# Performance work log

Measured on AMD Instinct MI355X. Metric: run time of the kernel, lower is better.

## Reference

```python
import jax, jax.numpy as jnp
import numpy as np

N = 262144          # number of input vectors (flattened tokens)
K = 1024            # codebook_size
D = 64              # embedding_dim
DECAY = 0.99
EPS = 1e-5
COMMIT = 0.25


def setup_inputs() -> dict:
    key = jax.random.key(0)
    k1, k2 = jax.random.split(key, 2)
    inputs = jax.random.normal(k1, (N, D), dtype=jnp.float32)
    # codebook.weight.data.normal_() -> standard normal init
    codebook = jax.random.normal(k2, (K, D), dtype=jnp.float32)
    ema_cluster_size = jnp.zeros((K,), dtype=jnp.float32)
    ema_w = codebook  # registered buffer initialized to a clone of the codebook
    return {"inputs": inputs, "codebook": codebook,
            "ema_cluster_size": ema_cluster_size, "ema_w": ema_w}


def reference(inputs, codebook, ema_cluster_size, ema_w):
    distances = (jnp.sum(inputs ** 2, axis=1, keepdims=True)
                 + jnp.sum(codebook ** 2, axis=1)
                 - 2.0 * (inputs @ codebook.T))
    encoding_indices = jnp.argmin(distances, axis=1)          # [N]

    # one_hot @ codebook  ==  gather
    quantized = codebook[encoding_indices]                    # [N, D]

    # --- training-mode EMA codebook update (buffers, no gradients) ---
    # encodings.sum(0)  ==  per-code counts
    counts = jax.ops.segment_sum(jnp.ones((inputs.shape[0],), inputs.dtype),
                                 encoding_indices, num_segments=K)
    new_cluster_size = DECAY * ema_cluster_size + (1.0 - DECAY) * counts
    n = jnp.sum(new_cluster_size)
    smoothed_size = (new_cluster_size + EPS) / (n + K * EPS) * n
    # encodings.T @ inputs  ==  segment sum of inputs by assigned code
    dw = jax.ops.segment_sum(inputs, encoding_indices, num_segments=K)  # [K, D]
    new_ema_w = DECAY * ema_w + (1.0 - DECAY) * dw
    new_codebook = new_ema_w / smoothed_size[:, None]

    # Straight-through estimator
    quantized_st = inputs + jax.lax.stop_gradient(quantized - inputs)
    e_latent_loss = jnp.mean((jax.lax.stop_gradient(quantized_st) - inputs) ** 2)
    loss = COMMIT * e_latent_loss

    return quantized_st, loss, encoding_indices, new_codebook, new_cluster_size, new_ema_w
```

## Files before the change

kernel.cpp:

```cpp
#include <hip/hip_runtime.h>

#define NN 262144
#define KK 1024
#define DD 64
#define DECAY 0.99f
#define ONE_MINUS_DECAY 0.01f
#define EPSF 1e-5f
#define COMMIT 0.25f

#define ROWB 144
#define CHUNK_CODES 32
#define PLANE_BYTES (CHUNK_CODES * ROWB)
#define CHUNK_BYTES (PLANE_BYTES * 2)
#define NCHUNK (KK / CHUNK_CODES)
#define RBLK 16384
#define CBLK 64
#define ROWS_PER_CBLK (NN / CBLK)

typedef __bf16 bf16x8 __attribute__((ext_vector_type(8)));
typedef unsigned short ushort8 __attribute__((ext_vector_type(8)));
typedef float float4v __attribute__((ext_vector_type(4)));

__device__ inline unsigned short bf16rne(float f) {
    unsigned int u = __float_as_uint(f);
    u += 0x7fffu + ((u >> 16) & 1u);
    return (unsigned short)(u >> 16);
}

__device__ inline void glds16(const void* g, void* l) {
    __builtin_amdgcn_global_load_lds(
        (const __attribute__((address_space(1))) unsigned int*)g,
        (__attribute__((address_space(3))) unsigned int*)l, 16, 0, 0);
}

__global__ __launch_bounds__(256) void k_prep(const float* __restrict__ cb,
                                              unsigned char* __restrict__ cbhl,
                                              float* __restrict__ csq_half,
                                              float* __restrict__ dw) {
    int e = blockIdx.x * 256 + threadIdx.x;
    dw[e] = 0.f;
    int k = e >> 6, d = e & 63;
    int c = k >> 5, kl = k & 31;
    float f = cb[e];
    unsigned short h = bf16rne(f);
    float hf = __uint_as_float((unsigned int)h << 16);
    unsigned short l = bf16rne(f - hf);
    unsigned char* base = cbhl + (size_t)c * CHUNK_BYTES;
    *(unsigned short*)(base + kl * ROWB + d * 2) = h;
    *(unsigned short*)(base + PLANE_BYTES + kl * ROWB + d * 2) = l;
    float s = f * f;
#pragma unroll
    for (int off = 32; off > 0; off >>= 1) s += __shfl_down(s, off);
    if (d == 0) csq_half[k] = 0.5f * s;
}

__global__ __launch_bounds__(256, 4) void k_assign(
    const float* __restrict__ x,
    const unsigned char* __restrict__ cbhl, const float* __restrict__ csq_half,
    int* __restrict__ kkpack)
{
    __shared__ __align__(16) unsigned char ldsbuf[2][CHUNK_BYTES];

    const int tid  = threadIdx.x;
    const int lane = tid & 63;
    const int wave = tid >> 6;
    const int col  = lane & 15;
    const int quad = lane >> 4;
    const int rowbase = blockIdx.x * 128 + wave * 32;

    {
        const unsigned char* src = cbhl;
#pragma unroll
        for (int i = 0; i < 2; ++i) {
            int off = (i * 256 + tid) * 16;
            glds16(src + off, &ldsbuf[0][off]);
        }
        if (tid < 64) {
            int off = 8192 + tid * 16;
            glds16(src + off, &ldsbuf[0][off]);
        }
    }

    bf16x8 nah[2][2], nal[2][2];
    float xsq1[8];
    {
        float xsqm[2];
#pragma unroll
        for (int mt = 0; mt < 2; ++mt) {
            const float* xb = x + (size_t)(rowbase + mt * 16 + col) * DD + quad * 8;
            float s = 0.f;
#pragma unroll
            for (int kh = 0; kh < 2; ++kh) {
                float4 f0 = *(const float4*)(xb + kh * 32);
                float4 f1 = *(const float4*)(xb + kh * 32 + 4);
                s += f0.x * f0.x + f0.y * f0.y + f0.z * f0.z + f0.w * f0.w;
                s += f1.x * f1.x + f1.y * f1.y + f1.z * f1.z + f1.w * f1.w;
                float fv[8] = {f0.x, f0.y, f0.z, f0.w, f1.x, f1.y, f1.z, f1.w};
                ushort8 uh, ul;
#pragma unroll
                for (int j = 0; j < 8; ++j) {
                    float nf = -fv[j];
                    unsigned short h = bf16rne(nf);
                    float hf = __uint_as_float((unsigned int)h << 16);
                    uh[j] = h;
                    ul[j] = bf16rne(nf - hf);
                }
                nah[mt][kh] = __builtin_bit_cast(bf16x8, uh);
                nal[mt][kh] = __builtin_bit_cast(bf16x8, ul);
            }
            s += __shfl_xor(s, 16);
            s += __shfl_xor(s, 32);
            xsqm[mt] = s;
        }
#pragma unroll
        for (int mt = 0; mt < 2; ++mt)
#pragma unroll
            for (int r = 0; r < 4; ++r)
                xsq1[mt * 4 + r] = 0.5f * __shfl(xsqm[mt], quad * 4 + r) + 1.0f;
    }

    unsigned int best[8], sec[8];
#pragma unroll
    for (int j = 0; j < 8; ++j) { best[j] = 0xFFFFFFFFu; sec[j] = 0xFFFFFFFFu; }

    asm volatile("s_waitcnt vmcnt(0) lgkmcnt(0)" ::: "memory");
    __builtin_amdgcn_s_barrier();

    for (int chunk = 0; chunk < NCHUNK; ++chunk) {
        const unsigned char* cbuf = ldsbuf[chunk & 1];
        if (chunk + 1 < NCHUNK) {
            unsigned char* nbuf = ldsbuf[(chunk + 1) & 1];
            const unsigned char* src = cbhl + (size_t)(chunk + 1) * CHUNK_BYTES;
#pragma unroll
            for (int i = 0; i < 2; ++i) {
                int off = (i * 256 + tid) * 16;
                glds16(src + off, nbuf + off);
            }
            if (tid < 64) {
                int off = 8192 + tid * 16;
                glds16(src + off, nbuf + off);
            }
        }

        float csqv[2];
#pragma unroll
        for (int ct = 0; ct < 2; ++ct)
            csqv[ct] = csq_half[chunk * CHUNK_CODES + ct * 16 + col];

#pragma unroll
        for (int ct = 0; ct < CHUNK_CODES / 16; ++ct) {
            const int code_local = ct * 16 + col;
            const unsigned int codeCol = chunk * CHUNK_CODES + code_local;
            const unsigned char* bp = cbuf + code_local * ROWB + quad * 16;
            bf16x8 bh0 = __builtin_bit_cast(bf16x8, *(const uint4*)(bp));
            bf16x8 bh1 = __builtin_bit_cast(bf16x8, *(const uint4*)(bp + 64));
            bf16x8 bl0 = __builtin_bit_cast(bf16x8, *(const uint4*)(bp + PLANE_BYTES));
            bf16x8 bl1 = __builtin_bit_cast(bf16x8, *(const uint4*)(bp + PLANE_BYTES + 64));
            float csq = csqv[ct];

#pragma unroll
            for (int mt = 0; mt < 2; ++mt) {
                float4v a = {csq + xsq1[mt * 4 + 0], csq + xsq1[mt * 4 + 1],
                             csq + xsq1[mt * 4 + 2], csq + xsq1[mt * 4 + 3]};
                __builtin_amdgcn_s_setprio(1);
                a = __builtin_amdgcn_mfma_f32_16x16x32_bf16(nah[mt][0], bh0, a, 0, 0, 0);
                a = __builtin_amdgcn_mfma_f32_16x16x32_bf16(nah[mt][1], bh1, a, 0, 0, 0);
                a = __builtin_amdgcn_mfma_f32_16x16x32_bf16(nah[mt][0], bl0, a, 0, 0, 0);
                a = __builtin_amdgcn_mfma_f32_16x16x32_bf16(nah[mt][1], bl1, a, 0, 0, 0);
                a = __builtin_amdgcn_mfma_f32_16x16x32_bf16(nal[mt][0], bh0, a, 0, 0, 0);
                a = __builtin_amdgcn_mfma_f32_16x16x32_bf16(nal[mt][1], bh1, a, 0, 0, 0);
                __builtin_amdgcn_s_setprio(0);
#pragma unroll
                for (int r = 0; r < 4; ++r) {
                    unsigned int u = (__float_as_uint(a[r]) & 0xFFFFFC00u) | codeCol;
                    unsigned int j = mt * 4 + r;
                    unsigned int s2;
                    asm("v_med3_u32 %0, %1, %2, %3"
                        : "=v"(s2) : "v"(best[j]), "v"(u), "v"(sec[j]));
                    sec[j] = s2;
                    best[j] = best[j] < u ? best[j] : u;
                }
            }
        }

        asm volatile("s_waitcnt vmcnt(0) lgkmcnt(0)" ::: "memory");
        __builtin_amdgcn_s_barrier();
    }

#pragma unroll
    for (int m = 1; m <= 8; m <<= 1) {
#pragma unroll
        for (int j = 0; j < 8; ++j) {
            unsigned int ob = __shfl_xor(best[j], m, 16);
            unsigned int os = __shfl_xor(sec[j],  m, 16);
            unsigned int hi = best[j] > ob ? best[j] : ob;
            best[j] = best[j] < ob ? best[j] : ob;
            unsigned int s2 = sec[j] < os ? sec[j] : os;
            sec[j] = s2 < hi ? s2 : hi;
        }
    }

    if (col == 0) {
#pragma unroll
        for (int j = 0; j < 8; ++j) {
            int row_local = (j >> 2) * 16 + quad * 4 + (j & 3);
            kkpack[rowbase + row_local] =
                (int)((best[j] & 1023u) | ((sec[j] & 1023u) << 10));
        }
    }
}

__global__ __launch_bounds__(256) void k_refine(
    const float* __restrict__ x, const float* __restrict__ cb,
    const float* __restrict__ csq_half, int* __restrict__ idx_io,
    float* __restrict__ quant, float* __restrict__ loss_parts)
{
    __shared__ float werr[4];
    const int tid  = threadIdx.x;
    const int lane = tid & 63;
    const int d16  = lane & 15;
    const int e    = blockIdx.x * 256 + tid;
    const int row  = e >> 4;

    unsigned int kp = (unsigned int)idx_io[row];
    int k1 = (int)(kp & 1023u), k2 = (int)((kp >> 10) & 1023u);

    float4 x4 = *(const float4*)(x + (size_t)row * DD + d16 * 4);
    float4 c1 = *(const float4*)(cb + (size_t)k1 * DD + d16 * 4);
    float4 c2 = *(const float4*)(cb + (size_t)k2 * DD + d16 * 4);

    float p1 = x4.x * c1.x + x4.y * c1.y + x4.z * c1.z + x4.w * c1.w;
    float p2 = x4.x * c2.x + x4.y * c2.y + x4.z * c2.z + x4.w * c2.w;
#pragma unroll
    for (int off = 1; off < 16; off <<= 1) {
        p1 += __shfl_xor(p1, off, 16);
        p2 += __shfl_xor(p2, off, 16);
    }
    float d1 = csq_half[k1] - p1;
    float d2 = csq_half[k2] - p2;
    bool pick1 = (d1 < d2) || (d1 == d2 && k1 < k2);
    int w = pick1 ? k1 : k2;
    float4 q = pick1 ? c1 : c2;

    *(float4*)(quant + (size_t)row * DD + d16 * 4) = q;

    float ex = q.x - x4.x, ey = q.y - x4.y, ez = q.z - x4.z, ew = q.w - x4.w;
    float err = ex * ex + ey * ey + ez * ez + ew * ew;
#pragma unroll
    for (int off = 32; off > 0; off >>= 1) err += __shfl_down(err, off);
    if (lane == 0) werr[tid >> 6] = err;
    __syncthreads();
    if (tid == 0)
        loss_parts[blockIdx.x] = werr[0] + werr[1] + werr[2] + werr[3];

    if (d16 == 0) idx_io[row] = w;
}

__global__ __launch_bounds__(1024) void k_count(
    const int* __restrict__ idx, int* __restrict__ counts_parts)
{
    __shared__ int hist[KK];
    const int tid = threadIdx.x;
    const int b   = blockIdx.x;
    hist[tid] = 0;
    __syncthreads();
    const int base = b * ROWS_PER_CBLK;
#pragma unroll
    for (int i = 0; i < ROWS_PER_CBLK / 1024; ++i)
        atomicAdd(&hist[idx[base + tid + i * 1024]], 1);
    __syncthreads();
    counts_parts[b * KK + tid] = hist[tid];
}

__global__ __launch_bounds__(1024) void k_mid(
    int* __restrict__ counts_parts, const float* __restrict__ ema_cs,
    const float* __restrict__ loss_parts,
    float* __restrict__ new_cs, float* __restrict__ loss_out,
    float* __restrict__ smoothed_inv)
{
    int t = threadIdx.x; int lane = t & 63; int w = t >> 6;

    __shared__ float wsumf[16];
    __shared__ int wsumi[16];
    __shared__ float wlp[16];
    __shared__ float ntot_s;

    float lp = 0.f;
#pragma unroll
    for (int i = 0; i < RBLK / 1024; ++i) lp += loss_parts[t + i * 1024];
#pragma unroll
    for (int off = 32; off > 0; off >>= 1) lp += __shfl_down(lp, off);
    if (lane == 0) wlp[w] = lp;

    int cnt = 0;
    for (int b = 0; b < CBLK; ++b) cnt += counts_parts[b * KK + t];
    float ncs = DECAY * ema_cs[t] + ONE_MINUS_DECAY * (float)cnt;

    float s = ncs;
#pragma unroll
    for (int off = 32; off > 0; off >>= 1) s += __shfl_down(s, off);
    if (lane == 0) wsumf[w] = s;

    int v = cnt;
#pragma unroll
    for (int off = 1; off < 64; off <<= 1) {
        int u = __shfl_up(v, off);
        if (lane >= off) v += u;
    }
    if (lane == 63) wsumi[w] = v;
    __syncthreads();
    if (t == 0) {
        float tt = 0.f, lt = 0.f;
        for (int i = 0; i < 16; ++i) { tt += wsumf[i]; lt += wlp[i]; }
        ntot_s = tt;
        loss_out[0] = COMMIT * lt / (float)(NN * DD);
    }
    if (w == 0 && lane < 16) {
        int u = wsumi[lane]; int vv = u;
#pragma unroll
        for (int off = 1; off < 16; off <<= 1) {
            int p = __shfl_up(vv, off, 16);
            if ((lane & 15) >= off) vv += p;
        }
        wsumi[lane] = vv - u;
    }
    __syncthreads();
    float n = ntot_s;

    float sm = (ncs + EPSF) / (n + (float)KK * EPSF) * n;
    new_cs[t] = ncs;
    smoothed_inv[t] = 1.0f / sm;

    int run = wsumi[w] + v - cnt;
    for (int b = 0; b < CBLK; ++b) {
        int c = counts_parts[b * KK + t];
        counts_parts[b * KK + t] = run;
        run += c;
    }
}

__global__ __launch_bounds__(1024) void k_scatter(
    int* __restrict__ idx_inout, const int* __restrict__ base_parts,
    int2* __restrict__ pairs)
{
    __shared__ int cur[KK];
    const int tid = threadIdx.x;
    const int b   = blockIdx.x;
    cur[tid] = base_parts[b * KK + tid];
    __syncthreads();
    const int base = b * ROWS_PER_CBLK;
#pragma unroll
    for (int i = 0; i < ROWS_PER_CBLK / 1024; ++i) {
        int r = base + tid + i * 1024;
        int k = idx_inout[r];
        int pos = atomicAdd(&cur[k], 1);
        pairs[pos] = make_int2(r, k);
        ((float*)idx_inout)[r] = (float)k;
    }
}

__global__ __launch_bounds__(256) void k_segsum(
    const float* __restrict__ x, const int2* __restrict__ pairs,
    float* __restrict__ dw)
{
    int w = blockIdx.x * 4 + (threadIdx.x >> 6);
    int lane = threadIdx.x & 63;
    int base = w * 64;
    int2 mine = pairs[base + lane];
    float acc = 0.f;
    int cur = __shfl(mine.y, 0);
    for (int rb = 0; rb < 64; rb += 8) {
        float v[8];
        int codes[8];
#pragma unroll
        for (int j = 0; j < 8; ++j) {
            int row  = __shfl(mine.x, rb + j);
            codes[j] = __shfl(mine.y, rb + j);
            v[j] = x[(size_t)row * DD + lane];
        }
#pragma unroll
        for (int j = 0; j < 8; ++j) {
            if (codes[j] != cur) {
                atomicAdd(&dw[cur * DD + lane], acc);
                acc = 0.f; cur = codes[j];
            }
            acc += v[j];
        }
    }
    atomicAdd(&dw[cur * DD + lane], acc);
}

__global__ __launch_bounds__(256) void k_final(
    const float* __restrict__ dw, const float* __restrict__ ema_w,
    const float* __restrict__ smoothed_inv,
    float* __restrict__ new_ema_w, float* __restrict__ new_cb)
{
    int i = blockIdx.x * 256 + threadIdx.x;
    int k = i >> 6;
    float nw = DECAY * ema_w[i] + ONE_MINUS_DECAY * dw[i];
    new_ema_w[i] = nw;
    new_cb[i] = nw * smoothed_inv[k];
}

extern "C" void kernel_launch(void* const* d_in, const int* in_sizes, int n_in,
                              void* d_out, int out_size, void* d_ws, size_t ws_size,
                              hipStream_t stream)
{
    const float* x      = (const float*)d_in[0];
    const float* cb     = (const float*)d_in[1];
    const float* ema_cs = (const float*)d_in[2];
    const float* ema_w  = (const float*)d_in[3];

    float* out      = (float*)d_out;
    float* quant    = out;
    float* loss_out = out + (size_t)NN * DD;
    int*   idx_reg  = (int*)(out + (size_t)NN * DD + 1);
    float* new_cb   = out + (size_t)NN * DD + 1 + NN;
    float* new_cs   = new_cb + (size_t)KK * DD;
    float* new_emaw = new_cs + KK;

    char* ws = (char*)d_ws;
    float* dw           = (float*)(ws + 4352);
    float* csq_half     = (float*)(ws + 274688);
    float* smoothed_inv = (float*)(ws + 278784);
    unsigned char* cbhl = (unsigned char*)(ws + 282880);
    int2*  pairs        = (int2*)(ws + 577792);
    int*   counts_parts = (int*)(ws + 282880);
    float* loss_parts   = (float*)(ws + 577792);

    k_prep   <<<KK * DD / 256, 256, 0, stream>>>(cb, cbhl, csq_half, dw);
    k_assign <<<NN / 128, 256, 0, stream>>>(x, cbhl, csq_half, idx_reg);
    k_refine <<<RBLK, 256, 0, stream>>>(x, cb, csq_half, idx_reg, quant,
                                        loss_parts);
    k_count  <<<CBLK, 1024, 0, stream>>>(idx_reg, counts_parts);
    k_mid    <<<1, 1024, 0, stream>>>(counts_parts, ema_cs, loss_parts,
                                      new_cs, loss_out, smoothed_inv);
    k_scatter<<<CBLK, 1024, 0, stream>>>(idx_reg, counts_parts, pairs);
    k_segsum <<<NN / 256, 256, 0, stream>>>(x, pairs, dw);
    k_final  <<<KK * DD / 256, 256, 0, stream>>>(dw, ema_w, smoothed_inv,
                                                 new_emaw, new_cb);
}
```

Measured before the change: 251.8 us.

## Switch assignment GEMM to 32x32x16 MFMA with MFMA-native codebook layout

Replaces the 16x16x32 bf16 MFMA tiling of the distance computation with 32x32x16 MFMAs. Each wave now covers 32 rows by 32 codes per chunk using 12 MFMAs on a 16-register accumulator. The codebook prep kernel writes the split-bf16 planes in a layout that matches the MFMA operand order, so each lane loads its fragments with contiguous 16-byte LDS reads and the padded rows go away. The change also drops the occupancy hint from the launch bounds, and the larger best/second-best state (16 registers each) raises register pressure.

New measurement: 270.0 us. 7.2% more time.

```diff
diff --git a/kernel.cpp b/kernel.cpp
--- a/kernel.cpp
+++ b/kernel.cpp
@@ -8,10 +8,9 @@
 #define EPSF 1e-5f
 #define COMMIT 0.25f
 
-#define ROWB 144
 #define CHUNK_CODES 32
-#define PLANE_BYTES (CHUNK_CODES * ROWB)
-#define CHUNK_BYTES (PLANE_BYTES * 2)
+#define PLANE_BYTES 4096
+#define CHUNK_BYTES 8192
 #define NCHUNK (KK / CHUNK_CODES)
 #define RBLK 16384
 #define CBLK 64
@@ -19,7 +18,7 @@
 
 typedef __bf16 bf16x8 __attribute__((ext_vector_type(8)));
 typedef unsigned short ushort8 __attribute__((ext_vector_type(8)));
-typedef float float4v __attribute__((ext_vector_type(4)));
+typedef float f32x16 __attribute__((ext_vector_type(16)));
 
 __device__ inline unsigned short bf16rne(float f) {
     unsigned int u = __float_as_uint(f);
@@ -40,21 +39,23 @@
     int e = blockIdx.x * 256 + threadIdx.x;
     dw[e] = 0.f;
     int k = e >> 6, d = e & 63;
-    int c = k >> 5, kl = k & 31;
+    int c = k >> 5, cl = k & 31;
+    int kb = d >> 4, hh = (d >> 3) & 1, j = d & 7;
     float f = cb[e];
-    unsigned short h = bf16rne(f);
-    float hf = __uint_as_float((unsigned int)h << 16);
-    unsigned short l = bf16rne(f - hf);
+    unsigned short h16 = bf16rne(f);
+    float hf = __uint_as_float((unsigned int)h16 << 16);
+    unsigned short l16 = bf16rne(f - hf);
     unsigned char* base = cbhl + (size_t)c * CHUNK_BYTES;
-    *(unsigned short*)(base + kl * ROWB + d * 2) = h;
-    *(unsigned short*)(base + PLANE_BYTES + kl * ROWB + d * 2) = l;
+    int off = kb * 1024 + hh * 512 + cl * 16 + j * 2;
+    *(unsigned short*)(base + off) = h16;
+    *(unsigned short*)(base + PLANE_BYTES + off) = l16;
     float s = f * f;
 #pragma unroll
-    for (int off = 32; off > 0; off >>= 1) s += __shfl_down(s, off);
+    for (int offr = 32; offr > 0; offr >>= 1) s += __shfl_down(s, offr);
     if (d == 0) csq_half[k] = 0.5f * s;
 }
 
-__global__ __launch_bounds__(256, 4) void k_assign(
+__global__ __launch_bounds__(256) void k_assign(
     const float* __restrict__ x,
     const unsigned char* __restrict__ cbhl, const float* __restrict__ csq_half,
     int* __restrict__ kkpack)
@@ -64,8 +65,8 @@
     const int tid  = threadIdx.x;
     const int lane = tid & 63;
     const int wave = tid >> 6;
-    const int col  = lane & 15;
-    const int quad = lane >> 4;
+    const int col  = lane & 31;
+    const int h    = lane >> 5;
     const int rowbase = blockIdx.x * 128 + wave * 32;
 
     {
@@ -75,53 +76,43 @@
             int off = (i * 256 + tid) * 16;
             glds16(src + off, &ldsbuf[0][off]);
         }
-        if (tid < 64) {
-            int off = 8192 + tid * 16;
-            glds16(src + off, &ldsbuf[0][off]);
-        }
-    }
-
-    bf16x8 nah[2][2], nal[2][2];
-    float xsq1[8];
+    }
+
+    bf16x8 nah[4], nal[4];
+    float xsq1[16];
     {
-        float xsqm[2];
-#pragma unroll
-        for (int mt = 0; mt < 2; ++mt) {
-            const float* xb = x + (size_t)(rowbase + mt * 16 + col) * DD + quad * 8;
-            float s = 0.f;
-#pragma unroll
-            for (int kh = 0; kh < 2; ++kh) {
-                float4 f0 = *(const float4*)(xb + kh * 32);
-                float4 f1 = *(const float4*)(xb + kh * 32 + 4);
-                s += f0.x * f0.x + f0.y * f0.y + f0.z * f0.z + f0.w * f0.w;
-                s += f1.x * f1.x + f1.y * f1.y + f1.z * f1.z + f1.w * f1.w;
-                float fv[8] = {f0.x, f0.y, f0.z, f0.w, f1.x, f1.y, f1.z, f1.w};
-                ushort8 uh, ul;
-#pragma unroll
-                for (int j = 0; j < 8; ++j) {
-                    float nf = -fv[j];
-                    unsigned short h = bf16rne(nf);
-                    float hf = __uint_as_float((unsigned int)h << 16);
-                    uh[j] = h;
-                    ul[j] = bf16rne(nf - hf);
-                }
-                nah[mt][kh] = __builtin_bit_cast(bf16x8, uh);
-                nal[mt][kh] = __builtin_bit_cast(bf16x8, ul);
+        const float* xr = x + (size_t)(rowbase + col) * DD + h * 8;
+        float s = 0.f;
+#pragma unroll
+        for (int kb = 0; kb < 4; ++kb) {
+            float4 f0 = *(const float4*)(xr + kb * 16);
+            float4 f1 = *(const float4*)(xr + kb * 16 + 4);
+            s += f0.x * f0.x + f0.y * f0.y + f0.z * f0.z + f0.w * f0.w;
+            s += f1.x * f1.x + f1.y * f1.y + f1.z * f1.z + f1.w * f1.w;
+            float fv[8] = {f0.x, f0.y, f0.z, f0.w, f1.x, f1.y, f1.z, f1.w};
+            ushort8 uh, ul;
+#pragma unroll
+            for (int j = 0; j < 8; ++j) {
+                float nf = -fv[j];
+                unsigned short hb = bf16rne(nf);
+                float hf = __uint_as_float((unsigned int)hb << 16);
+                uh[j] = hb;
+                ul[j] = bf16rne(nf - hf);
             }
-            s += __shfl_xor(s, 16);
-            s += __shfl_xor(s, 32);
-            xsqm[mt] = s;
-        }
-#pragma unroll
-        for (int mt = 0; mt < 2; ++mt)
-#pragma unroll
-            for (int r = 0; r < 4; ++r)
-                xsq1[mt * 4 + r] = 0.5f * __shfl(xsqm[mt], quad * 4 + r) + 1.0f;
-    }
-
-    unsigned int best[8], sec[8];
-#pragma unroll
-    for (int j = 0; j < 8; ++j) { best[j] = 0xFFFFFFFFu; sec[j] = 0xFFFFFFFFu; }
+            nah[kb] = __builtin_bit_cast(bf16x8, uh);
+            nal[kb] = __builtin_bit_cast(bf16x8, ul);
+        }
+        s += __shfl_xor(s, 32);
+#pragma unroll
+        for (int reg = 0; reg < 16; ++reg) {
+            int R = (reg & 3) + 8 * (reg >> 2) + 4 * h;
+            xsq1[reg] = 0.5f * __shfl(s, R) + 1.0f;
+        }
+    }
+
+    unsigned int best[16], sec[16];
+#pragma unroll
+    for (int j = 0; j < 16; ++j) { best[j] = 0xFFFFFFFFu; sec[j] = 0xFFFFFFFFu; }
 
     asm volatile("s_waitcnt vmcnt(0) lgkmcnt(0)" ::: "memory");
     __builtin_amdgcn_s_barrier();
@@ -136,51 +127,44 @@
                 int off = (i * 256 + tid) * 16;
                 glds16(src + off, nbuf + off);
             }
-            if (tid < 64) {
-                int off = 8192 + tid * 16;
-                glds16(src + off, nbuf + off);
-            }
-        }
-
-        float csqv[2];
-#pragma unroll
-        for (int ct = 0; ct < 2; ++ct)
-            csqv[ct] = csq_half[chunk * CHUNK_CODES + ct * 16 + col];
-
-#pragma unroll
-        for (int ct = 0; ct < CHUNK_CODES / 16; ++ct) {
-            const int code_local = ct * 16 + col;
-            const unsigned int codeCol = chunk * CHUNK_CODES + code_local;
-            const unsigned char* bp = cbuf + code_local * ROWB + quad * 16;
-            bf16x8 bh0 = __builtin_bit_cast(bf16x8, *(const uint4*)(bp));
-            bf16x8 bh1 = __builtin_bit_cast(bf16x8, *(const uint4*)(bp + 64));
-            bf16x8 bl0 = __builtin_bit_cast(bf16x8, *(const uint4*)(bp + PLANE_BYTES));
-            bf16x8 bl1 = __builtin_bit_cast(bf16x8, *(const uint4*)(bp + PLANE_BYTES + 64));
-            float csq = csqv[ct];
-
-#pragma unroll
-            for (int mt = 0; mt < 2; ++mt) {
-                float4v a = {csq + xsq1[mt * 4 + 0], csq + xsq1[mt * 4 + 1],
-                             csq + xsq1[mt * 4 + 2], csq + xsq1[mt * 4 + 3]};
-                __builtin_amdgcn_s_setprio(1);
-                a = __builtin_amdgcn_mfma_f32_16x16x32_bf16(nah[mt][0], bh0, a, 0, 0, 0);
-                a = __builtin_amdgcn_mfma_f32_16x16x32_bf16(nah[mt][1], bh1, a, 0, 0, 0);
-                a = __builtin_amdgcn_mfma_f32_16x16x32_bf16(nah[mt][0], bl0, a, 0, 0, 0);
-                a = __builtin_amdgcn_mfma_f32_16x16x32_bf16(nah[mt][1], bl1, a, 0, 0, 0);
-                a = __builtin_amdgcn_mfma_f32_16x16x32_bf16(nal[mt][0], bh0, a, 0, 0, 0);
-                a = __builtin_amdgcn_mfma_f32_16x16x32_bf16(nal[mt][1], bh1, a, 0, 0, 0);
-                __builtin_amdgcn_s_setprio(0);
-#pragma unroll
-                for (int r = 0; r < 4; ++r) {
-                    unsigned int u = (__float_as_uint(a[r]) & 0xFFFFFC00u) | codeCol;
-                    unsigned int j = mt * 4 + r;
-                    unsigned int s2;
-                    asm("v_med3_u32 %0, %1, %2, %3"
-                        : "=v"(s2) : "v"(best[j]), "v"(u), "v"(sec[j]));
-                    sec[j] = s2;
-                    best[j] = best[j] < u ? best[j] : u;
-                }
-            }
+        }
+
+        float csq = csq_half[chunk * CHUNK_CODES + col];
+        const unsigned int codeCol = chunk * CHUNK_CODES + col;
+
+        bf16x8 bh[4], bl[4];
+#pragma unroll
+        for (int kb = 0; kb < 4; ++kb) {
+            bh[kb] = __builtin_bit_cast(bf16x8,
+                *(const uint4*)(cbuf + kb * 1024 + lane * 16));
+            bl[kb] = __builtin_bit_cast(bf16x8,
+                *(const uint4*)(cbuf + PLANE_BYTES + kb * 1024 + lane * 16));
+        }
+
+        f32x16 a;
+#pragma unroll
+        for (int reg = 0; reg < 16; ++reg) a[reg] = csq + xsq1[reg];
+
+        __builtin_amdgcn_s_setprio(1);
+#pragma unroll
+        for (int kb = 0; kb < 4; ++kb)
+            a = __builtin_amdgcn_mfma_f32_32x32x16_bf16(nah[kb], bh[kb], a, 0, 0, 0);
+#pragma unroll
+        for (int kb = 0; kb < 4; ++kb)
+            a = __builtin_amdgcn_mfma_f32_32x32x16_bf16(nah[kb], bl[kb], a, 0, 0, 0);
+#pragma unroll
+        for (int kb = 0; kb < 4; ++kb)
+            a = __builtin_amdgcn_mfma_f32_32x32x16_bf16(nal[kb], bh[kb], a, 0, 0, 0);
+        __builtin_amdgcn_s_setprio(0);
+
+#pragma unroll
+        for (int reg = 0; reg < 16; ++reg) {
+            unsigned int u = (__float_as_uint(a[reg]) & 0xFFFFFC00u) | codeCol;
+            unsigned int s2;
+            asm("v_med3_u32 %0, %1, %2, %3"
+                : "=v"(s2) : "v"(best[reg]), "v"(u), "v"(sec[reg]));
+            sec[reg] = s2;
+            best[reg] = best[reg] < u ? best[reg] : u;
         }
 
         asm volatile("s_waitcnt vmcnt(0) lgkmcnt(0)" ::: "memory");
@@ -188,24 +172,24 @@
     }
 
 #pragma unroll
-    for (int m = 1; m <= 8; m <<= 1) {
-#pragma unroll
-        for (int j = 0; j < 8; ++j) {
-            unsigned int ob = __shfl_xor(best[j], m, 16);
-            unsigned int os = __shfl_xor(sec[j],  m, 16);
-            unsigned int hi = best[j] > ob ? best[j] : ob;
-            best[j] = best[j] < ob ? best[j] : ob;
-            unsigned int s2 = sec[j] < os ? sec[j] : os;
-            sec[j] = s2 < hi ? s2 : hi;
+    for (int m = 1; m <= 16; m <<= 1) {
+#pragma unroll
+        for (int reg = 0; reg < 16; ++reg) {
+            unsigned int ob = __shfl_xor(best[reg], m);
+            unsigned int os = __shfl_xor(sec[reg], m);
+            unsigned int hi = best[reg] > ob ? best[reg] : ob;
+            best[reg] = best[reg] < ob ? best[reg] : ob;
+            unsigned int s2 = sec[reg] < os ? sec[reg] : os;
+            sec[reg] = s2 < hi ? s2 : hi;
         }
     }
 
     if (col == 0) {
 #pragma unroll
-        for (int j = 0; j < 8; ++j) {
-            int row_local = (j >> 2) * 16 + quad * 4 + (j & 3);
+        for (int reg = 0; reg < 16; ++reg) {
+            int row_local = (reg & 3) + 8 * (reg >> 2) + 4 * h;
             kkpack[rowbase + row_local] =
-                (int)((best[j] & 1023u) | ((sec[j] & 1023u) << 10));
+                (int)((best[reg] & 1023u) | ((sec[reg] & 1023u) << 10));
         }
     }
 }
```
